# Kernel tuning notes

Measured on AMD Instinct MI355X. Metric: run time of the kernel, lower is better.

The kernel has to match this reference:

```python
import jax, jax.numpy as jnp
import numpy as np

D_MODEL = 512
NUM_HEADS = 8
D_K = D_MODEL // NUM_HEADS


def setup_inputs() -> dict:
    key = jax.random.key(0)
    ks = jax.random.split(key, 9)
    B, S = 2, 2048
    s = 1.0 / np.sqrt(D_MODEL)
    x = jax.random.normal(ks[0], (B, S, D_MODEL), dtype=jnp.float32)
    Wq = jax.random.uniform(ks[1], (D_MODEL, D_MODEL), jnp.float32, -s, s)
    bq = jax.random.uniform(ks[2], (D_MODEL,), jnp.float32, -s, s)
    Wk = jax.random.uniform(ks[3], (D_MODEL, D_MODEL), jnp.float32, -s, s)
    bk = jax.random.uniform(ks[4], (D_MODEL,), jnp.float32, -s, s)
    Wv = jax.random.uniform(ks[5], (D_MODEL, D_MODEL), jnp.float32, -s, s)
    bv = jax.random.uniform(ks[6], (D_MODEL,), jnp.float32, -s, s)
    Wo = jax.random.uniform(ks[7], (D_MODEL, D_MODEL), jnp.float32, -s, s)
    bo = jax.random.uniform(ks[8], (D_MODEL,), jnp.float32, -s, s)
    return {"x": x, "Wq": Wq, "bq": bq, "Wk": Wk, "bk": bk,
            "Wv": Wv, "bv": bv, "Wo": Wo, "bo": bo}


def reference(x, Wq, bq, Wk, bk, Wv, bv, Wo, bo):
    B, S, _ = x.shape
    # QKV projections -> [B, H, S, d_k]
    def proj(W, b):
        return (x @ W + b).reshape(B, S, NUM_HEADS, D_K).transpose(0, 2, 1, 3)
    q = proj(Wq, bq)
    k = proj(Wk, bk)
    v = proj(Wv, bv)
    # Full [B, H, S, S] scores (faithful to the original unfused attention)
    scores = jnp.einsum('bhqd,bhkd->bhqk', q, k) / jnp.sqrt(jnp.float32(D_K))
    attn = jax.nn.softmax(scores, axis=-1)  # dropout is identity in eval mode
    context = jnp.einsum('bhqk,bhkd->bhqd', attn, v)
    context = context.transpose(0, 2, 1, 3).reshape(B, S, D_MODEL)
    return context @ Wo + bo
```

## Files before the change

### kernel.cpp

```cpp
#include <hip/hip_runtime.h>
#include <hip/hip_bf16.h>

typedef __attribute__((ext_vector_type(8))) short bf16x8_t;
typedef __attribute__((ext_vector_type(4))) short short4_t;
typedef __attribute__((ext_vector_type(4))) float f32x4_t;
typedef __hip_bfloat16 bf16;

#define DM    512
#define SEQ   2048
#define NH    8
#define DKH   64
#define MTOT  4096
#define QBLK  64
#define KVBLK 128
#define QSCALE 0.180336884f

__device__ __forceinline__ bf16x8_t frag16_swz(const bf16* sm, int row, int stride_b, int kbyte) {
    const int b = (row * stride_b + kbyte) ^ ((row & 7) << 4);
    return *(const bf16x8_t*)((const char*)sm + b);
}

__device__ __forceinline__ bf16x8_t frag8_swz(const bf16* sm, int row, int stride_b, int ebase) {
    const int s  = (row & 7) << 4;
    const char* p = (const char*)sm;
    const int b0 = (row * stride_b + ebase * 2) ^ s;
    const int b1 = (row * stride_b + ebase * 2 + 32) ^ s;
    short4_t lo = *(const short4_t*)(p + b0);
    short4_t hi = *(const short4_t*)(p + b1);
    return __builtin_shufflevector(lo, hi, 0, 1, 2, 3, 4, 5, 6, 7);
}

__device__ __forceinline__ void gload_lds16(const bf16* g, bf16* s) {
    __builtin_amdgcn_global_load_lds(
        (const __attribute__((address_space(1))) unsigned int*)g,
        (__attribute__((address_space(3))) unsigned int*)s, 16, 0, 0);
}

__device__ __forceinline__ bf16x8_t pack_pa(const f32x4_t a, const f32x4_t b) {
    bf16 t[8];
    #pragma unroll
    for (int j = 0; j < 4; ++j) t[j]     = __float2bfloat16(a[j]);
    #pragma unroll
    for (int j = 0; j < 4; ++j) t[4 + j] = __float2bfloat16(b[j]);
    return *(bf16x8_t*)t;
}

__device__ __forceinline__ short4_t cvt4(const f32x4_t v, float scale) {
    short4_t r;
    #pragma unroll
    for (int i = 0; i < 4; ++i) ((bf16*)&r)[i] = __float2bfloat16(v[i] * scale);
    return r;
}

__global__ __launch_bounds__(256) void prep(
    const float* __restrict__ x,
    const float* __restrict__ Wq, const float* __restrict__ Wk,
    const float* __restrict__ Wv, const float* __restrict__ Wo,
    bf16* __restrict__ WT, bf16* __restrict__ Xb)
{
    __shared__ bf16 t[32][33];
    const int z = blockIdx.z, tid = threadIdx.x;
    if (z < 4) {
        const float* W = (z == 0) ? Wq : (z == 1) ? Wk : (z == 2) ? Wv : Wo;
        bf16* T = WT + (size_t)z * DM * DM;
        const int tx = tid & 31, ty = tid >> 5;
        const int x0 = blockIdx.x * 32, y0 = blockIdx.y * 32;
        #pragma unroll
        for (int i = ty; i < 32; i += 8)
            t[i][tx] = __float2bfloat16(W[(size_t)(y0 + i) * DM + x0 + tx]);
        __syncthreads();
        #pragma unroll
        for (int i = ty; i < 32; i += 8)
            T[(size_t)(x0 + i) * DM + y0 + tx] = t[tx][i];
    } else {
        const int base = (blockIdx.y * 16 + blockIdx.x) * 256 + tid;
        #pragma unroll
        for (int j = 0; j < 8; ++j) {
            const int t4 = base + j * 65536;
            const float4 v = ((const float4*)x)[t4];
            bf16 o[4] = { __float2bfloat16(v.x), __float2bfloat16(v.y),
                          __float2bfloat16(v.z), __float2bfloat16(v.w) };
            ((short4_t*)Xb)[t4] = *(short4_t*)o;
        }
    }
}

__device__ __forceinline__ void stage128(
    const bf16* __restrict__ A, const bf16* __restrict__ Bt,
    int rowBase, int colBase, int kb, bf16* Asm, bf16* Bsm, int tid)
{
    #pragma unroll
    for (int j = 0; j < 4; ++j) {
        const int c = tid + 256 * j;
        const int row = c >> 3, cc = (((c & 7) ^ (row & 7)) << 3);
        gload_lds16(&A [(size_t)(rowBase + row) * DM + kb + cc], Asm + c * 8);
        gload_lds16(&Bt[(size_t)(colBase + row) * DM + kb + cc], Bsm + c * 8);
    }
}

__device__ __forceinline__ void gemm128_core(
    const bf16* __restrict__ A, const bf16* __restrict__ Bt,
    int rowBase, int colBase, bf16* sm, f32x4_t acc[4][4])
{
    const int tid = threadIdx.x;
    const int w = tid >> 6, l = tid & 63, lg = l >> 4, lr = l & 15;
    const int wm = w >> 1, wn = w & 1;

    stage128(A, Bt, rowBase, colBase, 0, sm, sm + 16384, tid);
    __syncthreads();

    int cur = 0;
    for (int t = 0; t < DM / 64; ++t) {
        if (t < DM / 64 - 1)
            stage128(A, Bt, rowBase, colBase, (t + 1) * 64,
                     sm + (cur ^ 1) * 8192, sm + 16384 + (cur ^ 1) * 8192, tid);
        const bf16* Asm = sm + cur * 8192;
        const bf16* Bsm = sm + 16384 + cur * 8192;
        #pragma unroll
        for (int ks = 0; ks < 2; ++ks) {
            bf16x8_t af[4], bfr[4];
            #pragma unroll
            for (int m = 0; m < 4; ++m) af[m]  = frag16_swz(Asm, wm * 64 + m * 16 + lr, 128, ks * 64 + lg * 16);
            #pragma unroll
            for (int n = 0; n < 4; ++n) bfr[n] = frag16_swz(Bsm, wn * 64 + n * 16 + lr, 128, ks * 64 + lg * 16);
            #pragma unroll
            for (int m = 0; m < 4; ++m)
                #pragma unroll
                for (int n = 0; n < 4; ++n)
                    acc[m][n] = __builtin_amdgcn_mfma_f32_16x16x32_bf16(af[m], bfr[n], acc[m][n], 0, 0, 0);
        }
        __syncthreads();
        cur ^= 1;
    }
}

__global__ __launch_bounds__(256) void qkv_proj(
    const bf16* __restrict__ X, const bf16* __restrict__ WTall,
    const float* __restrict__ bq, const float* __restrict__ bk, const float* __restrict__ bv,
    bf16* __restrict__ Qo, bf16* __restrict__ Ko, bf16* __restrict__ Vto)
{
    __shared__ bf16 sm[32768];
    f32x4_t acc[4][4] = {};
    const int rowBase = blockIdx.y * 128, colBase = blockIdx.x * 128;
    gemm128_core(X, WTall, rowBase, colBase, sm, acc);

    const int tid = threadIdx.x, w = tid >> 6, l = tid & 63, lg = l >> 4, lr = l & 15;
    const int wm = w >> 1, wn = w & 1;
    #pragma unroll
    for (int n = 0; n < 4; ++n) {
        const int c = colBase + wn * 64 + n * 16 + lr;
        const int z = c >> 9, cc = c & 511, h = cc >> 6, d = cc & 63;
        const float bb = (z == 0 ? bq : z == 1 ? bk : bv)[cc];
        #pragma unroll
        for (int m = 0; m < 4; ++m) {
            const int r0 = rowBase + wm * 64 + m * 16 + lg * 4;
            const int b = r0 >> 11, s0 = r0 & 2047;
            if (z == 2) {
                f32x4_t v = acc[m][n];
                #pragma unroll
                for (int i = 0; i < 4; ++i) v[i] += bb;
                *(short4_t*)&Vto[(((size_t)(b * NH + h)) * DKH + d) * SEQ + s0] = cvt4(v, 1.0f);
            } else {
                #pragma unroll
                for (int i = 0; i < 4; ++i) {
                    const float v = acc[m][n][i] + bb;
                    if (z == 0)
                        Qo[(((size_t)(b * NH + h)) * SEQ + s0 + i) * DKH + d] = __float2bfloat16(v * QSCALE);
                    else
                        Ko[(((size_t)(b * NH + h)) * SEQ + s0 + i) * DKH + d] = __float2bfloat16(v);
                }
            }
        }
    }
}

__global__ __launch_bounds__(256) void attn(
    const bf16* __restrict__ Q, const bf16* __restrict__ K,
    const bf16* __restrict__ VT, bf16* __restrict__ Ctx)
{
    __shared__ bf16 sm[4 * 8192];

    const int bh = blockIdx.y;
    const int qb = blockIdx.x * QBLK;
    const int tid = threadIdx.x, w = tid >> 6, l = tid & 63, lg = l >> 4, lr = l & 15;
    const size_t hbase = (size_t)bh * SEQ * DKH;
    const bf16* Qh = Q + hbase;
    const bf16* Kh = K + hbase;
    const bf16* Vh = VT + hbase;

    bf16x8_t qf[2];
    {
        const bf16* qp = Qh + (size_t)(qb + w * 16 + lr) * DKH;
        qf[0] = *(const bf16x8_t*)(qp + lg * 8);
        qf[1] = *(const bf16x8_t*)(qp + 32 + lg * 8);
    }

    bf16x8_t ones;
    #pragma unroll
    for (int j = 0; j < 8; ++j) ones[j] = (short)0x3F80;

    f32x4_t Oacc[4] = {};
    f32x4_t lacc = {};

    const int kr = tid >> 3, kc = (((tid & 7) ^ (kr & 7)) << 3);
    const int vr = tid >> 4, vc = (((tid & 15) ^ (vr & 7)) << 3);

    #pragma unroll
    for (int j = 0; j < 4; ++j)
        gload_lds16(&Kh[(size_t)(kr + 32 * j) * DKH + kc], sm + (tid + 256 * j) * 8);
    #pragma unroll
    for (int j = 0; j < 4; ++j)
        gload_lds16(&Vh[(size_t)(vr + 16 * j) * SEQ + vc], sm + 16384 + (tid + 256 * j) * 8);
    __syncthreads();

    int cur = 0;
    for (int t = 0; t < SEQ / KVBLK; ++t) {
        bf16* Kc = sm + cur * 8192;
        bf16* Vc = sm + 16384 + cur * 8192;

        if (t < SEQ / KVBLK - 1) {
            const int kb = (t + 1) * KVBLK;
            bf16* Kn = sm + (cur ^ 1) * 8192;
            bf16* Vn = sm + 16384 + (cur ^ 1) * 8192;
            #pragma unroll
            for (int j = 0; j < 4; ++j)
                gload_lds16(&Kh[(size_t)(kb + kr + 32 * j) * DKH + kc], Kn + (tid + 256 * j) * 8);
            #pragma unroll
            for (int j = 0; j < 4; ++j)
                gload_lds16(&Vh[(size_t)(vr + 16 * j) * SEQ + kb + vc], Vn + (tid + 256 * j) * 8);
        }

        f32x4_t sacc[8] = {};
        #pragma unroll
        for (int nf = 0; nf < 8; ++nf) {
            const int r = nf * 16 + lr;
            bf16x8_t k0 = frag16_swz(Kc, r, 128, lg * 16);
            bf16x8_t k1 = frag16_swz(Kc, r, 128, 64 + lg * 16);
            sacc[nf] = __builtin_amdgcn_mfma_f32_16x16x32_bf16(k0, qf[0], sacc[nf], 0, 0, 0);
            sacc[nf] = __builtin_amdgcn_mfma_f32_16x16x32_bf16(k1, qf[1], sacc[nf], 0, 0, 0);
        }

        #pragma unroll
        for (int nf = 0; nf < 8; ++nf)
            #pragma unroll
            for (int i = 0; i < 4; ++i) sacc[nf][i] = exp2f(sacc[nf][i]);

        #pragma unroll
        for (int ks = 0; ks < 4; ++ks) {
            const bf16x8_t pf = pack_pa(sacc[2 * ks], sacc[2 * ks + 1]);
            lacc = __builtin_amdgcn_mfma_f32_16x16x32_bf16(ones, pf, lacc, 0, 0, 0);
            #pragma unroll
            for (int nf = 0; nf < 4; ++nf) {
                bf16x8_t vf = frag8_swz(Vc, nf * 16 + lr, 256, ks * 32 + lg * 4);
                Oacc[nf] = __builtin_amdgcn_mfma_f32_16x16x32_bf16(vf, pf, Oacc[nf], 0, 0, 0);
            }
        }

        __syncthreads();
        cur ^= 1;
    }

    const int b = bh >> 3, h = bh & 7;
    const float inv = 1.0f / lacc[0];
    const int s = qb + w * 16 + lr;
    bf16* cp = Ctx + (((size_t)b * SEQ + s) * NH + h) * DKH + lg * 4;
    #pragma unroll
    for (int nf = 0; nf < 4; ++nf)
        *(short4_t*)(cp + nf * 16) = cvt4(Oacc[nf], inv);
}

__global__ __launch_bounds__(256) void out_proj(
    const bf16* __restrict__ X, const bf16* __restrict__ Bt,
    const float* __restrict__ bias, float* __restrict__ Out)
{
    __shared__ bf16 sm[32768];
    f32x4_t acc[4][4] = {};
    const int rowBase = blockIdx.y * 128, colBase = blockIdx.x * 128;
    gemm128_core(X, Bt, rowBase, colBase, sm, acc);

    const int tid = threadIdx.x, w = tid >> 6, l = tid & 63, lg = l >> 4, lr = l & 15;
    const int wm = w >> 1, wn = w & 1;
    #pragma unroll
    for (int n = 0; n < 4; ++n) {
        const int c = colBase + wn * 64 + n * 16 + lr;
        const float bb = bias[c];
        #pragma unroll
        for (int m = 0; m < 4; ++m)
            #pragma unroll
            for (int i = 0; i < 4; ++i) {
                const int r = rowBase + wm * 64 + m * 16 + lg * 4 + i;
                Out[(size_t)r * DM + c] = acc[m][n][i] + bb;
            }
    }
}

extern "C" void kernel_launch(void* const* d_in, const int* in_sizes, int n_in,
                              void* d_out, int out_size, void* d_ws, size_t ws_size,
                              hipStream_t stream) {
    const float* x  = (const float*)d_in[0];
    const float* Wq = (const float*)d_in[1];
    const float* bq = (const float*)d_in[2];
    const float* Wk = (const float*)d_in[3];
    const float* bk = (const float*)d_in[4];
    const float* Wv = (const float*)d_in[5];
    const float* bv = (const float*)d_in[6];
    const float* Wo = (const float*)d_in[7];
    const float* bo = (const float*)d_in[8];
    float* out = (float*)d_out;

    bf16* ws  = (bf16*)d_ws;
    bf16* WT  = ws;
    bf16* Xb  = ws + 1048576;
    bf16* Qw  = ws + 1048576 + 1 * 2097152;
    bf16* Kw  = ws + 1048576 + 2 * 2097152;
    bf16* VTw = ws + 1048576 + 3 * 2097152;
    bf16* Ctx = ws + 1048576 + 4 * 2097152;

    prep<<<dim3(16, 16, 5), 256, 0, stream>>>(x, Wq, Wk, Wv, Wo, WT, Xb);
    qkv_proj<<<dim3(12, 32), 256, 0, stream>>>(Xb, WT, bq, bk, bv, Qw, Kw, VTw);
    attn<<<dim3(SEQ / QBLK, 16), 256, 0, stream>>>(Qw, Kw, VTw, Ctx);
    out_proj<<<dim3(4, 32), 256, 0, stream>>>(Ctx, WT + (size_t)3 * DM * DM, bo, out);
}
```

Before: 132.7 us.

## Process two 16-row query groups per warp in attention to reuse K/V fragments

Doubles the query block to 128 rows so each warp handles two 16-row query groups. K and V fragments read from LDS are reused across both groups, halving the shared-memory reads and global K/V loads per query row. The trade-off is higher register pressure (a launch-bounds occupancy hint is added) and half as many blocks, which reduces grid parallelism to 16 blocks per head.

```diff
diff --git a/kernel.cpp b/kernel.cpp
--- a/kernel.cpp
+++ b/kernel.cpp
@@ -11,7 +11,7 @@
 #define NH    8
 #define DKH   64
 #define MTOT  4096
-#define QBLK  64
+#define QBLK  128
 #define KVBLK 128
 #define QSCALE 0.180336884f
 
@@ -174,7 +174,7 @@
     }
 }
 
-__global__ __launch_bounds__(256) void attn(
+__global__ __launch_bounds__(256, 2) void attn(
     const bf16* __restrict__ Q, const bf16* __restrict__ K,
     const bf16* __restrict__ VT, bf16* __restrict__ Ctx)
 {
@@ -188,19 +188,20 @@
     const bf16* Kh = K + hbase;
     const bf16* Vh = VT + hbase;
 
-    bf16x8_t qf[2];
-    {
-        const bf16* qp = Qh + (size_t)(qb + w * 16 + lr) * DKH;
-        qf[0] = *(const bf16x8_t*)(qp + lg * 8);
-        qf[1] = *(const bf16x8_t*)(qp + 32 + lg * 8);
+    bf16x8_t qf[2][2];
+    #pragma unroll
+    for (int g = 0; g < 2; ++g) {
+        const bf16* qp = Qh + (size_t)(qb + w * 32 + g * 16 + lr) * DKH;
+        qf[g][0] = *(const bf16x8_t*)(qp + lg * 8);
+        qf[g][1] = *(const bf16x8_t*)(qp + 32 + lg * 8);
     }
 
     bf16x8_t ones;
     #pragma unroll
     for (int j = 0; j < 8; ++j) ones[j] = (short)0x3F80;
 
-    f32x4_t Oacc[4] = {};
-    f32x4_t lacc = {};
+    f32x4_t Oacc[2][4] = {};
+    f32x4_t lacc[2] = {};
 
     const int kr = tid >> 3, kc = (((tid & 7) ^ (kr & 7)) << 3);
     const int vr = tid >> 4, vc = (((tid & 15) ^ (vr & 7)) << 3);
@@ -230,29 +231,40 @@
                 gload_lds16(&Vh[(size_t)(vr + 16 * j) * SEQ + kb + vc], Vn + (tid + 256 * j) * 8);
         }
 
-        f32x4_t sacc[8] = {};
+        f32x4_t sacc[2][8] = {};
         #pragma unroll
         for (int nf = 0; nf < 8; ++nf) {
             const int r = nf * 16 + lr;
             bf16x8_t k0 = frag16_swz(Kc, r, 128, lg * 16);
             bf16x8_t k1 = frag16_swz(Kc, r, 128, 64 + lg * 16);
-            sacc[nf] = __builtin_amdgcn_mfma_f32_16x16x32_bf16(k0, qf[0], sacc[nf], 0, 0, 0);
-            sacc[nf] = __builtin_amdgcn_mfma_f32_16x16x32_bf16(k1, qf[1], sacc[nf], 0, 0, 0);
-        }
-
-        #pragma unroll
-        for (int nf = 0; nf < 8; ++nf)
-            #pragma unroll
-            for (int i = 0; i < 4; ++i) sacc[nf][i] = exp2f(sacc[nf][i]);
+            #pragma unroll
+            for (int g = 0; g < 2; ++g) {
+                sacc[g][nf] = __builtin_amdgcn_mfma_f32_16x16x32_bf16(k0, qf[g][0], sacc[g][nf], 0, 0, 0);
+                sacc[g][nf] = __builtin_amdgcn_mfma_f32_16x16x32_bf16(k1, qf[g][1], sacc[g][nf], 0, 0, 0);
+            }
+        }
+
+        #pragma unroll
+        for (int g = 0; g < 2; ++g)
+            #pragma unroll
+            for (int nf = 0; nf < 8; ++nf)
+                #pragma unroll
+                for (int i = 0; i < 4; ++i) sacc[g][nf][i] = exp2f(sacc[g][nf][i]);
 
         #pragma unroll
         for (int ks = 0; ks < 4; ++ks) {
-            const bf16x8_t pf = pack_pa(sacc[2 * ks], sacc[2 * ks + 1]);
-            lacc = __builtin_amdgcn_mfma_f32_16x16x32_bf16(ones, pf, lacc, 0, 0, 0);
+            bf16x8_t pf[2];
+            #pragma unroll
+            for (int g = 0; g < 2; ++g) {
+                pf[g] = pack_pa(sacc[g][2 * ks], sacc[g][2 * ks + 1]);
+                lacc[g] = __builtin_amdgcn_mfma_f32_16x16x32_bf16(ones, pf[g], lacc[g], 0, 0, 0);
+            }
             #pragma unroll
             for (int nf = 0; nf < 4; ++nf) {
                 bf16x8_t vf = frag8_swz(Vc, nf * 16 + lr, 256, ks * 32 + lg * 4);
-                Oacc[nf] = __builtin_amdgcn_mfma_f32_16x16x32_bf16(vf, pf, Oacc[nf], 0, 0, 0);
+                #pragma unroll
+                for (int g = 0; g < 2; ++g)
+                    Oacc[g][nf] = __builtin_amdgcn_mfma_f32_16x16x32_bf16(vf, pf[g], Oacc[g][nf], 0, 0, 0);
             }
         }
 
@@ -261,12 +273,15 @@
     }
 
     const int b = bh >> 3, h = bh & 7;
-    const float inv = 1.0f / lacc[0];
-    const int s = qb + w * 16 + lr;
-    bf16* cp = Ctx + (((size_t)b * SEQ + s) * NH + h) * DKH + lg * 4;
-    #pragma unroll
-    for (int nf = 0; nf < 4; ++nf)
-        *(short4_t*)(cp + nf * 16) = cvt4(Oacc[nf], inv);
+    #pragma unroll
+    for (int g = 0; g < 2; ++g) {
+        const float inv = 1.0f / lacc[g][0];
+        const int s = qb + w * 32 + g * 16 + lr;
+        bf16* cp = Ctx + (((size_t)b * SEQ + s) * NH + h) * DKH + lg * 4;
+        #pragma unroll
+        for (int nf = 0; nf < 4; ++nf)
+            *(short4_t*)(cp + nf * 16) = cvt4(Oacc[g][nf], inv);
+    }
 }
 
 __global__ __launch_bounds__(256) void out_proj(
```

Result: no change. 134.4 us (+1.3%).
